# Performance work log

Hardware: AMD Instinct MI355X
Metric: run time of the kernel (lower is better)

Reference implementation:

```python
import jax, jax.numpy as jnp
import numpy as np

N = 300000   # number of occupied voxels (sparse tensor rows)
L = 100      # grid side length -> 1e6 cells, occupancy 0.3
C = 32       # channels (channelwise/depthwise conv)
KS = 3       # kernel_size per axis
D = 3        # spatial dimension
R = (KS - 1) // 2


def _build_sparse_structure():
    """Sample N unique voxel coords and build kernel maps (edge lists) like
    MinkowskiEngine's coordinate manager: for each kernel offset, pairs
    (in_idx, out_idx) such that coords[in_idx] == coords[out_idx] + offset."""
    rng = np.random.default_rng(0)
    flat = rng.choice(L ** 3, size=N, replace=False)
    coords = np.stack([flat // (L * L), (flat // L) % L, flat % L], axis=1).astype(np.int32)
    keys = flat.astype(np.int64)
    order = np.argsort(keys)
    sk = keys[order]
    out_ids = np.arange(N, dtype=np.int64)
    in_list, out_list = [], []
    for dx in range(-R, R + 1):
        for dy in range(-R, R + 1):
            for dz in range(-R, R + 1):
                nx = coords[:, 0].astype(np.int64) + dx
                ny = coords[:, 1].astype(np.int64) + dy
                nz = coords[:, 2].astype(np.int64) + dz
                inb = (nx >= 0) & (nx < L) & (ny >= 0) & (ny < L) & (nz >= 0) & (nz < L)
                nk = (nx * L + ny) * L + nz
                pos = np.searchsorted(sk, nk)
                pos_c = np.clip(pos, 0, N - 1)
                ok = inb & (sk[pos_c] == nk)
                in_list.append(order[pos_c[ok]])
                out_list.append(out_ids[ok])
    in_idx = np.concatenate(in_list).astype(np.int32)
    out_idx = np.concatenate(out_list).astype(np.int32)
    return coords, in_idx, out_idx


def setup_inputs() -> dict:
    coords, in_idx, out_idx = _build_sparse_structure()
    key = jax.random.key(0)
    k1, k2 = jax.random.split(key)
    in_feats = jax.random.normal(k1, (N, C), dtype=jnp.float32)
    kernel = jax.random.normal(k2, (KS ** D, C), dtype=jnp.float32)  # depthwise kernel
    return {
        "coords": jnp.asarray(coords),
        "in_idx": jnp.asarray(in_idx),
        "out_idx": jnp.asarray(out_idx),
        "in_feats": in_feats,
        "kernel": kernel,
    }


def reference(coords, in_idx, out_idx, in_feats, kernel):
    # index_array = KS ** flip(arange(D)) -> [9, 3, 1] for KS=3, D=3
    index_pow = jnp.array([KS ** (D - 1 - i) for i in range(D)], dtype=jnp.int32)
    # tensor_stride = 1; kernel_coord = (C_in - C_out)//1 + (KS-1)//2, per edge [E, D]
    kernel_coord = coords[in_idx] - coords[out_idx] + R
    k1d = jnp.sum(index_pow[None, :] * kernel_coord, axis=1)  # [E] in [0, KS**D)
    # gather-multiply-scatter: out_F[out] += in_feats[in] * kernel[k1d]
    out_F = jnp.zeros_like(in_feats).at[out_idx].add(in_feats[in_idx] * kernel[k1d])
    return out_F
```

## Files before the change

### kernel.cpp

```cpp
#include <hip/hip_runtime.h>

#define NCH 32
#define GROUPS 8
#define KVOL 27
#define LG 100
#define LP 102
#define RGN 5
#define NRGN 20
#define NREGIONS (NRGN * NRGN * NRGN)
#define BSIDE 7
#define BVOL 343
#define CELLS 125
#define LSTR 28

__global__ void build_dense(const int* __restrict__ coords,
                            int* __restrict__ dense, int N) {
    int i = blockIdx.x * blockDim.x + threadIdx.x;
    if (i >= N) return;
    int x = coords[3 * i + 0];
    int y = coords[3 * i + 1];
    int z = coords[3 * i + 2];
    dense[((size_t)(x + 1) * LP + (y + 1)) * LP + (z + 1)] = i + 1;
}

__global__ __launch_bounds__(256) void gather_conv_region(
        const int* __restrict__ dense,
        const float4* __restrict__ in_feats4,
        const float4* __restrict__ kernel4,
        float4* __restrict__ out4) {
    __shared__ float4 kw[(KVOL + 1) * GROUPS];
    __shared__ int brick[BVOL];
    __shared__ int qmeta[CELLS];
    __shared__ int smap[CELLS];
    __shared__ int hist[7];
    __shared__ __align__(16) unsigned int list[CELLS * LSTR];
    __shared__ int nint;

    int tid = threadIdx.x;
    int g   = tid & 7;

    if (tid == 0) nint = 0;
    if (tid < 7) hist[tid] = 0;
    if (tid < (KVOL + 1) * GROUPS) {
        int kr = tid >> 3;
        kw[tid] = (kr < KVOL) ? kernel4[tid]
                              : make_float4(0.f, 0.f, 0.f, 0.f);
    }

    int b = blockIdx.x;
    int r = (b & 7) * (NREGIONS >> 3) + (b >> 3);
    int bx = r / (NRGN * NRGN);
    int by = (r / NRGN) % NRGN;
    int bz = r % NRGN;
    int ox = bx * RGN, oy = by * RGN, oz = bz * RGN;

    for (int i = tid; i < BVOL; i += 256) {
        int lx = i / 49, ly = (i / 7) % 7, lz = i % 7;
        int v = dense[((size_t)(ox + lx) * LP + (oy + ly)) * LP + (oz + lz)];
        brick[i] = v;
        if (v && (unsigned)(lx - 1) < RGN && (unsigned)(ly - 1) < RGN &&
            (unsigned)(lz - 1) < RGN) {
            int p = atomicAdd(&nint, 1);
            qmeta[p] = i;
        }
    }
    __syncthreads();

    int n = nint;

    int oct = tid >> 3, l = tid & 7;
    int rounds = (n + 31) >> 5;
    for (int rd = 0; rd < rounds; ++rd) {
        int q = (rd << 5) + oct;
        bool valid = q < n;
        int cell = valid ? (qmeta[q] & 511) : 0;
        int cnt = 0;
        unsigned base = (unsigned)q * LSTR;
        #pragma unroll
        for (int s = 0; s < 4; ++s) {
            int k = l + (s << 3);
            int nb = 0;
            if (valid && k < KVOL) {
                int off = (k / 9) * 49 + ((k / 3) % 3) * 7 + (k % 3) - 57;
                nb = brick[cell + off];
            }
            unsigned long long bal = __ballot(nb > 0);
            int byte = (int)((bal >> ((oct & 7) << 3)) & 0xFF);
            if (nb > 0) {
                int pos = cnt + __popc(byte & ((1 << l) - 1));
                list[base + pos] =
                    ((unsigned)(nb - 1) << 13) | ((unsigned)k << 7);
            }
            cnt += __popc(byte);
        }
        if (valid && l == 0) {
            int j = cnt;
            unsigned dummy =
                ((unsigned)(brick[cell] - 1) << 13) | (27u << 7);
            while (j & 3) list[base + (j++)] = dummy;
            int nq = j >> 2;
            int h = atomicAdd(&hist[nq - 1], 1);
            qmeta[q] = cell | (nq << 9) | (h << 12);
        }
    }
    __syncthreads();

    if (tid < n) {
        int m  = qmeta[tid];
        int nq = (m >> 9) & 7;
        int pos = m >> 12;
        #pragma unroll
        for (int bb = 1; bb < 7; ++bb)
            if (bb >= nq) pos += hist[bb];
        smap[pos] = (tid << 4) | nq;
    }
    __syncthreads();

    const char* kwb = (const char*)kw + (g << 4);
    int lr = tid >> 3;
    for (int base = 0; base < n; base += 32) {
        int lo = base + lr;
        if (lo < n) {
            int d    = smap[lo];
            int q    = d >> 4;
            int nq   = d & 15;
            int orow = brick[qmeta[q] & 511] - 1;
            const uint4* tl = (const uint4*)&list[(unsigned)q * LSTR];
            float4 acc = make_float4(0.f, 0.f, 0.f, 0.f);
            for (int jq = 0; jq < nq; ++jq) {
                uint4 L = tl[jq];
                float4 f0 = in_feats4[(size_t)(L.x >> 13) * GROUPS + g];
                float4 f1 = in_feats4[(size_t)(L.y >> 13) * GROUPS + g];
                float4 f2 = in_feats4[(size_t)(L.z >> 13) * GROUPS + g];
                float4 f3 = in_feats4[(size_t)(L.w >> 13) * GROUPS + g];
                float4 w0 = *(const float4*)(kwb + (L.x & 0x1F80u));
                float4 w1 = *(const float4*)(kwb + (L.y & 0x1F80u));
                float4 w2 = *(const float4*)(kwb + (L.z & 0x1F80u));
                float4 w3 = *(const float4*)(kwb + (L.w & 0x1F80u));
                acc.x += f0.x * w0.x; acc.y += f0.y * w0.y;
                acc.z += f0.z * w0.z; acc.w += f0.w * w0.w;
                acc.x += f1.x * w1.x; acc.y += f1.y * w1.y;
                acc.z += f1.z * w1.z; acc.w += f1.w * w1.w;
                acc.x += f2.x * w2.x; acc.y += f2.y * w2.y;
                acc.z += f2.z * w2.z; acc.w += f2.w * w2.w;
                acc.x += f3.x * w3.x; acc.y += f3.y * w3.y;
                acc.z += f3.z * w3.z; acc.w += f3.w * w3.w;
            }
            out4[(size_t)orow * GROUPS + g] = acc;
        }
    }
}

__global__ void mink_conv_scatter(const int* __restrict__ coords,
                                  const int* __restrict__ in_idx,
                                  const int* __restrict__ out_idx,
                                  const float4* __restrict__ in_feats4,
                                  const float4* __restrict__ kernel4,
                                  float* __restrict__ out,
                                  int E) {
    __shared__ float4 kws[KVOL * GROUPS];
    for (int i = threadIdx.x; i < KVOL * GROUPS; i += blockDim.x)
        kws[i] = kernel4[i];
    __syncthreads();
    int t = blockIdx.x * blockDim.x + threadIdx.x;
    if (t >= E * GROUPS) return;
    int e = t >> 3, g = t & 7;
    int vi = in_idx[e], vo = out_idx[e];
    int c0 = coords[vi * 3 + 0] - coords[vo * 3 + 0] + 1;
    int c1 = coords[vi * 3 + 1] - coords[vo * 3 + 1] + 1;
    int c2 = coords[vi * 3 + 2] - coords[vo * 3 + 2] + 1;
    int k1d = (c0 * 3 + c1) * 3 + c2;
    float4 f = in_feats4[vi * GROUPS + g];
    float4 w = kws[k1d * GROUPS + g];
    float* o = out + vo * NCH + g * 4;
    atomicAdd(o + 0, f.x * w.x);
    atomicAdd(o + 1, f.y * w.y);
    atomicAdd(o + 2, f.z * w.z);
    atomicAdd(o + 3, f.w * w.w);
}

extern "C" void kernel_launch(void* const* d_in, const int* in_sizes, int n_in,
                              void* d_out, int out_size, void* d_ws, size_t ws_size,
                              hipStream_t stream) {
    const int*   coords   = (const int*)d_in[0];
    const int*   in_idx   = (const int*)d_in[1];
    const int*   out_idx  = (const int*)d_in[2];
    const float* in_feats = (const float*)d_in[3];
    const float* kernel   = (const float*)d_in[4];

    const int E     = in_sizes[1];
    const int Nrows = out_size / NCH;

    const size_t dense_bytes = (size_t)LP * LP * LP * sizeof(int);

    if (ws_size >= dense_bytes) {
        int* dense = (int*)d_ws;
        hipMemsetAsync(dense, 0, dense_bytes, stream);

        int block = 256;
        int grid1 = (Nrows + block - 1) / block;
        build_dense<<<grid1, block, 0, stream>>>(coords, dense, Nrows);

        gather_conv_region<<<NREGIONS, 256, 0, stream>>>(
            dense, (const float4*)in_feats, (const float4*)kernel,
            (float4*)d_out);
    } else {
        hipMemsetAsync(d_out, 0, (size_t)out_size * sizeof(float), stream);
        int total = E * GROUPS;
        int block = 256;
        int grid  = (total + block - 1) / block;
        mink_conv_scatter<<<grid, block, 0, stream>>>(
            coords, in_idx, out_idx,
            (const float4*)in_feats, (const float4*)kernel,
            (float*)d_out, E);
    }
}
```

Baseline: 135.8 us.

## Replace per-cell neighbor lists with occupancy bitmasks decoded in the compute loop

Removes the large shared neighbor-list array and builds a 27-bit neighbor occupancy mask per output cell from column bitmaps filled with atomicOr. The compute loop decodes the mask with ctz and looks up the brick and kernel offsets on the fly. Cutting shared memory allows a higher occupancy hint (launch bounds 256,8), and smap is permuted so lanes in an 8-row group take work of similar length. The cost is extra bit manipulation and shared-memory lookups inside the inner loop.

```diff
diff --git a/kernel.cpp b/kernel.cpp
--- a/kernel.cpp
+++ b/kernel.cpp
@@ -11,7 +11,6 @@
 #define BSIDE 7
 #define BVOL 343
 #define CELLS 125
-#define LSTR 28
 
 __global__ void build_dense(const int* __restrict__ coords,
                             int* __restrict__ dense, int N) {
@@ -23,17 +22,19 @@
     dense[((size_t)(x + 1) * LP + (y + 1)) * LP + (z + 1)] = i + 1;
 }
 
-__global__ __launch_bounds__(256) void gather_conv_region(
+__global__ __launch_bounds__(256, 8) void gather_conv_region(
         const int* __restrict__ dense,
         const float4* __restrict__ in_feats4,
         const float4* __restrict__ kernel4,
         float4* __restrict__ out4) {
     __shared__ float4 kw[(KVOL + 1) * GROUPS];
     __shared__ int brick[BVOL];
+    __shared__ unsigned bitcol[49];
     __shared__ int qmeta[CELLS];
+    __shared__ unsigned qmask[CELLS];
     __shared__ int smap[CELLS];
+    __shared__ unsigned koff[KVOL + 1];
     __shared__ int hist[7];
-    __shared__ __align__(16) unsigned int list[CELLS * LSTR];
     __shared__ int nint;
 
     int tid = threadIdx.x;
@@ -41,6 +42,14 @@
 
     if (tid == 0) nint = 0;
     if (tid < 7) hist[tid] = 0;
+    if (tid < 49) bitcol[tid] = 0;
+    if (tid < KVOL + 1) {
+        int k = tid;
+        int dx = 1, dy = 1, dz = 1;
+        if (k < KVOL) { dx = k / 9; dy = (k / 3) % 3; dz = k % 3; }
+        int off = dx * 49 + dy * 7 + dz;
+        koff[tid] = ((unsigned)(k * 128) << 7) | (unsigned)off;
+    }
     if (tid < (KVOL + 1) * GROUPS) {
         int kr = tid >> 3;
         kw[tid] = (kr < KVOL) ? kernel4[tid]
@@ -58,61 +67,49 @@
         int lx = i / 49, ly = (i / 7) % 7, lz = i % 7;
         int v = dense[((size_t)(ox + lx) * LP + (oy + ly)) * LP + (oz + lz)];
         brick[i] = v;
-        if (v && (unsigned)(lx - 1) < RGN && (unsigned)(ly - 1) < RGN &&
-            (unsigned)(lz - 1) < RGN) {
-            int p = atomicAdd(&nint, 1);
-            qmeta[p] = i;
+        if (v) {
+            atomicOr(&bitcol[lx * 7 + ly], 1u << lz);
+            if ((unsigned)(lx - 1) < RGN && (unsigned)(ly - 1) < RGN &&
+                (unsigned)(lz - 1) < RGN) {
+                int p = atomicAdd(&nint, 1);
+                qmeta[p] = lx | (ly << 3) | (lz << 6) | (i << 9);
+            }
         }
     }
     __syncthreads();
 
     int n = nint;
 
-    int oct = tid >> 3, l = tid & 7;
-    int rounds = (n + 31) >> 5;
-    for (int rd = 0; rd < rounds; ++rd) {
-        int q = (rd << 5) + oct;
-        bool valid = q < n;
-        int cell = valid ? (qmeta[q] & 511) : 0;
-        int cnt = 0;
-        unsigned base = (unsigned)q * LSTR;
+    if (tid < n) {
+        int m0 = qmeta[tid];
+        int lx = m0 & 7, ly = (m0 >> 3) & 7, lz = (m0 >> 6) & 7;
+        int colbase = (lx - 1) * 7 + (ly - 1);
+        unsigned mask = 0;
         #pragma unroll
-        for (int s = 0; s < 4; ++s) {
-            int k = l + (s << 3);
-            int nb = 0;
-            if (valid && k < KVOL) {
-                int off = (k / 9) * 49 + ((k / 3) % 3) * 7 + (k % 3) - 57;
-                nb = brick[cell + off];
+        for (int dx = 0; dx < 3; ++dx)
+            #pragma unroll
+            for (int dy = 0; dy < 3; ++dy) {
+                unsigned c = (bitcol[colbase + dx * 7 + dy] >> (lz - 1)) & 7u;
+                mask |= c << (dx * 9 + dy * 3);
             }
-            unsigned long long bal = __ballot(nb > 0);
-            int byte = (int)((bal >> ((oct & 7) << 3)) & 0xFF);
-            if (nb > 0) {
-                int pos = cnt + __popc(byte & ((1 << l) - 1));
-                list[base + pos] =
-                    ((unsigned)(nb - 1) << 13) | ((unsigned)k << 7);
-            }
-            cnt += __popc(byte);
-        }
-        if (valid && l == 0) {
-            int j = cnt;
-            unsigned dummy =
-                ((unsigned)(brick[cell] - 1) << 13) | (27u << 7);
-            while (j & 3) list[base + (j++)] = dummy;
-            int nq = j >> 2;
-            int h = atomicAdd(&hist[nq - 1], 1);
-            qmeta[q] = cell | (nq << 9) | (h << 12);
-        }
+        qmask[tid] = mask;
+        int nb = (__popc(mask) + 3) >> 2;
+        int h = atomicAdd(&hist[nb - 1], 1);
+        qmeta[tid] = m0 | (nb << 18) | (h << 22);
     }
     __syncthreads();
 
     if (tid < n) {
-        int m  = qmeta[tid];
-        int nq = (m >> 9) & 7;
-        int pos = m >> 12;
+        int m0 = qmeta[tid];
+        int nb = (m0 >> 18) & 15;
+        int pos = m0 >> 22;
         #pragma unroll
         for (int bb = 1; bb < 7; ++bb)
-            if (bb >= nq) pos += hist[bb];
-        smap[pos] = (tid << 4) | nq;
+            if (bb >= nb) pos += hist[bb];
+        int s = pos;
+        if (pos < (n & ~31))
+            s = (pos & ~31) | ((pos >> 2) & 7) | ((pos & 3) << 3);
+        smap[s] = (tid << 5) | nb;
     }
     __syncthreads();
 
@@ -121,22 +118,34 @@
     for (int base = 0; base < n; base += 32) {
         int lo = base + lr;
         if (lo < n) {
-            int d    = smap[lo];
-            int q    = d >> 4;
-            int nq   = d & 15;
-            int orow = brick[qmeta[q] & 511] - 1;
-            const uint4* tl = (const uint4*)&list[(unsigned)q * LSTR];
+            int d     = smap[lo];
+            int q     = d >> 5;
+            int nb    = d & 31;
+            int m0    = qmeta[q];
+            int cell  = (m0 >> 9) & 511;
+            int cellb = cell - 57;
+            int orow  = brick[cell] - 1;
+            unsigned m = qmask[q];
             float4 acc = make_float4(0.f, 0.f, 0.f, 0.f);
-            for (int jq = 0; jq < nq; ++jq) {
-                uint4 L = tl[jq];
-                float4 f0 = in_feats4[(size_t)(L.x >> 13) * GROUPS + g];
-                float4 f1 = in_feats4[(size_t)(L.y >> 13) * GROUPS + g];
-                float4 f2 = in_feats4[(size_t)(L.z >> 13) * GROUPS + g];
-                float4 f3 = in_feats4[(size_t)(L.w >> 13) * GROUPS + g];
-                float4 w0 = *(const float4*)(kwb + (L.x & 0x1F80u));
-                float4 w1 = *(const float4*)(kwb + (L.y & 0x1F80u));
-                float4 w2 = *(const float4*)(kwb + (L.z & 0x1F80u));
-                float4 w3 = *(const float4*)(kwb + (L.w & 0x1F80u));
+            for (int t = 0; t < nb; ++t) {
+                int k0 = m ? __builtin_ctz(m) : KVOL; m &= m - 1;
+                int k1 = m ? __builtin_ctz(m) : KVOL; m &= m - 1;
+                int k2 = m ? __builtin_ctz(m) : KVOL; m &= m - 1;
+                int k3 = m ? __builtin_ctz(m) : KVOL; m &= m - 1;
+                unsigned o0 = koff[k0], o1 = koff[k1];
+                unsigned o2 = koff[k2], o3 = koff[k3];
+                int v0 = brick[cellb + (int)(o0 & 127u)];
+                int v1 = brick[cellb + (int)(o1 & 127u)];
+                int v2 = brick[cellb + (int)(o2 & 127u)];
+                int v3 = brick[cellb + (int)(o3 & 127u)];
+                float4 f0 = in_feats4[(size_t)(v0 - 1) * GROUPS + g];
+                float4 f1 = in_feats4[(size_t)(v1 - 1) * GROUPS + g];
+                float4 f2 = in_feats4[(size_t)(v2 - 1) * GROUPS + g];
+                float4 f3 = in_feats4[(size_t)(v3 - 1) * GROUPS + g];
+                float4 w0 = *(const float4*)(kwb + (o0 >> 7));
+                float4 w1 = *(const float4*)(kwb + (o1 >> 7));
+                float4 w2 = *(const float4*)(kwb + (o2 >> 7));
+                float4 w3 = *(const float4*)(kwb + (o3 >> 7));
                 acc.x += f0.x * w0.x; acc.y += f0.y * w0.y;
                 acc.z += f0.z * w0.z; acc.w += f0.w * w0.w;
                 acc.x += f1.x * w1.x; acc.y += f1.y * w1.y;
```

New measurement: 136.6 us. Within noise of the previous version (+0.6%).
